# Kernel optimization log

Hardware: AMD Instinct MI355X
Metric: run time of the kernel (lower is better)

## Reference

```python
import jax, jax.numpy as jnp
import numpy as np

BETA = 0.95
THR = 1.0
SLOPE = 25.0


@jax.custom_vjp
def spike(x):
    # Heaviside spike with fast-sigmoid surrogate gradient (snntorch fast_sigmoid, slope=25)
    return (x > 0).astype(x.dtype)

def _spike_fwd(x):
    return spike(x), x

def _spike_bwd(x, g):
    sg = 1.0 / (SLOPE * jnp.abs(x) + 1.0) ** 2
    return (g * sg,)

spike.defvjp(_spike_fwd, _spike_bwd)


def setup_inputs() -> dict:
    key = jax.random.key(0)
    k_x, k_w1, k_b1, k_w2, k_b2 = jax.random.split(key, 5)
    T, B, D_IN, H, OUT = 30, 4096, 784, 128, 10
    x = jax.random.uniform(k_x, (T, B, D_IN), dtype=jnp.float32)
    # PyTorch nn.Linear default init: U(-1/sqrt(fan_in), 1/sqrt(fan_in))
    lim1 = 1.0 / np.sqrt(D_IN)
    lim2 = 1.0 / np.sqrt(H)
    W1 = jax.random.uniform(k_w1, (H, D_IN), jnp.float32, -lim1, lim1)
    b1 = jax.random.uniform(k_b1, (H,), jnp.float32, -lim1, lim1)
    W2 = jax.random.uniform(k_w2, (OUT, H), jnp.float32, -lim2, lim2)
    b2 = jax.random.uniform(k_b2, (OUT,), jnp.float32, -lim2, lim2)
    return {"x": x, "W1": W1, "b1": b1, "W2": W2, "b2": b2}


def reference(x, W1, b1, W2, b2):
    T, B, _ = x.shape
    H, OUT = W1.shape[0], W2.shape[0]

    def step(carry, xt):
        mem1, mem2 = carry
        # layer 1: linear + leaky integrate-and-fire (reset by subtraction)
        cur1 = xt @ W1.T + b1  # [B, H]
        reset1 = jax.lax.stop_gradient((mem1 - THR > 0).astype(xt.dtype))
        mem1 = BETA * mem1 + cur1 - reset1 * THR
        spk1 = spike(mem1 - THR)
        # layer 2
        cur2 = spk1 @ W2.T + b2  # [B, OUT]
        reset2 = jax.lax.stop_gradient((mem2 - THR > 0).astype(xt.dtype))
        mem2 = BETA * mem2 + cur2 - reset2 * THR
        spk2 = spike(mem2 - THR)
        return (mem1, mem2), (spk2, mem2)

    init = (jnp.zeros((B, H), x.dtype), jnp.zeros((B, OUT), x.dtype))
    _, (spk2_rec, mem2_rec) = jax.lax.scan(step, init, x)
    return spk2_rec, mem2_rec  # each [T, B, OUT]
```

## Files before the change

### kernel.cpp

```cpp
#include <hip/hip_runtime.h>
#include <stdint.h>

#define THR  1.0f
#define BETA 0.95f
#define SX   4096.0f
#define SW   512.0f
#define SINV (1.0f / (4096.0f * 512.0f))
#define W1N  (128 * 784)

typedef __attribute__((ext_vector_type(8)))  _Float16 f16x8;
typedef __attribute__((ext_vector_type(16))) float    f32x16;
typedef __attribute__((ext_vector_type(4)))  float    fvec4;

__device__ __forceinline__ void gll16(const float* g, float* l){
  __builtin_amdgcn_global_load_lds((const __attribute__((address_space(1))) void*)g,
                                   (__attribute__((address_space(3))) void*)l, 16, 0, 0);
}

__global__ void split_w1(const float* __restrict__ W1, _Float16* __restrict__ wB){
  int i = blockIdx.x * 256 + threadIdx.x;
  if (i < W1N) {
    int h = i / 784, k = i % 784;
    float v = W1[i] * SW;
    _Float16 hi = (_Float16)v;
    _Float16 lo = (_Float16)(v - (float)hi);
    int ks = k >> 4, kg = (k >> 3) & 1, j = k & 7, nf = h >> 5, r = h & 31;
    int base = ((ks * 4 + nf) * 2) * 512 + (kg * 32 + r) * 8 + j;
    wB[base]       = hi;
    wB[base + 512] = lo;
  }
}

__launch_bounds__(256, 2)
__global__ void gemm1(const float* __restrict__ x,
                      const float* __restrict__ wBf,
                      const float* __restrict__ b1,
                      float* __restrict__ cur1,
                      long row0){
  __shared__ float lds[20480];
  const int lane = threadIdx.x & 63;
  const int w    = threadIdx.x >> 6;
  const long blk_row0 = row0 + (long)blockIdx.x * 128;
  const int r  = lane & 31;
  const int kg = lane >> 5;

  const float* xA  = x + (blk_row0 + w * 32 + r) * 784 + kg * 8;
  const float* wBs = wBf + w * 512 + lane * 4;

  #define STAGE(bb, s) {                                                     \
    gll16(xA  + (s) * 16,         &lds[(bb) * 4096 + (w * 2 + 0) * 256]);    \
    gll16(xA  + (s) * 16 + 4,     &lds[(bb) * 4096 + (w * 2 + 1) * 256]);    \
    gll16(wBs + (s) * 2048,       &lds[(bb) * 4096 + 2048 + (w * 2 + 0) * 256]); \
    gll16(wBs + (s) * 2048 + 256, &lds[(bb) * 4096 + 2048 + (w * 2 + 1) * 256]); }

  #define CPH(bb) {                                                          \
    f16x8 b[8];                                                              \
    _Pragma("unroll") for (int f = 0; f < 8; ++f)                            \
      b[f] = *(const f16x8*)&lds[(bb) * 4096 + 2048 + f * 256 + lane * 4];   \
    fvec4 a0 = *(const fvec4*)&lds[(bb) * 4096 + (w * 2 + 0) * 256 + lane * 4]; \
    fvec4 a1 = *(const fvec4*)&lds[(bb) * 4096 + (w * 2 + 1) * 256 + lane * 4]; \
    f16x8 ah, al;                                                            \
    _Pragma("unroll") for (int j = 0; j < 8; ++j) {                          \
      float v = ((j < 4) ? a0[j] : a1[j - 4]) * SX;                          \
      _Float16 hh = (_Float16)v;                                             \
      ah[j] = hh; al[j] = (_Float16)(v - (float)hh);                         \
    }                                                                        \
    _Pragma("unroll") for (int nf = 0; nf < 4; ++nf) {                       \
      acc[nf] = __builtin_amdgcn_mfma_f32_32x32x16_f16(ah, b[nf * 2],     acc[nf], 0, 0, 0); \
      acc[nf] = __builtin_amdgcn_mfma_f32_32x32x16_f16(ah, b[nf * 2 + 1], acc[nf], 0, 0, 0); \
      acc[nf] = __builtin_amdgcn_mfma_f32_32x32x16_f16(al, b[nf * 2],     acc[nf], 0, 0, 0); \
    } }

  #define VMB(vm) {                                                          \
    asm volatile("s_waitcnt vmcnt(" #vm ")" ::: "memory");                   \
    __builtin_amdgcn_s_barrier();                                            \
    asm volatile("" ::: "memory");                                           \
    __builtin_amdgcn_sched_barrier(0); }

  f32x16 acc[4] = {};

  STAGE(0, 0); STAGE(1, 1); STAGE(2, 2);

  for (int g = 0; g < 9; ++g) {
    const int s5 = 5 * g;
    STAGE(3, s5 + 3); VMB(12); CPH(0);
    STAGE(4, s5 + 4); VMB(12); CPH(1);
    STAGE(0, s5 + 5); VMB(12); CPH(2);
    STAGE(1, s5 + 6); VMB(12); CPH(3);
    STAGE(2, s5 + 7); VMB(12); CPH(4);
  }
  STAGE(3, 48); VMB(12); CPH(0);
  VMB(8);  CPH(1);
  VMB(4);  CPH(2);
  VMB(0);  CPH(3);

  float b1v[4];
  #pragma unroll
  for (int nf = 0; nf < 4; ++nf) b1v[nf] = b1[nf * 32 + r];
  long m0 = (long)blockIdx.x * 128 + w * 32;
  #pragma unroll
  for (int nf = 0; nf < 4; ++nf)
    #pragma unroll
    for (int reg = 0; reg < 16; ++reg) {
      int rr = (reg & 3) + 8 * (reg >> 2) + 4 * kg;
      cur1[(m0 + rr) * 128 + nf * 32 + r] = acc[nf][reg] * SINV + b1v[nf];
    }
  #undef STAGE
  #undef CPH
  #undef VMB
}

__launch_bounds__(256)
__global__ void lif(const float* __restrict__ cur1,
                    const float* __restrict__ W2,
                    const float* __restrict__ b2,
                    float* __restrict__ out,
                    float* __restrict__ state1,
                    float* __restrict__ state2,
                    int t0, int tn){
  const int lane = threadIdx.x & 63;
  const int b = blockIdx.x * 4 + (threadIdx.x >> 6);
  const int o = lane & 15;
  const int c = lane >> 4;

  float wv[32];
  #pragma unroll
  for (int j = 0; j < 32; ++j) wv[j] = 0.f;
  if (o < 10) {
    #pragma unroll
    for (int j = 0; j < 32; ++j) wv[j] = W2[o * 128 + c * 32 + j];
  }
  float b2v = (lane < 10) ? b2[lane] : 0.f;

  float mem1a, mem1b, mem2;
  if (t0 == 0) { mem1a = 0.f; mem1b = 0.f; mem2 = 0.f; }
  else {
    mem1a = state1[b * 128 + lane];
    mem1b = state1[b * 128 + 64 + lane];
    mem2  = (lane < 10) ? state2[b * 10 + lane] : 0.f;
  }

  for (int t = t0; t < tn; ++t) {
    long base = ((long)(t - t0) * 4096 + b) * 128;
    float c1a = cur1[base + lane];
    float c1b = cur1[base + 64 + lane];
    float r1a = (mem1a > THR) ? THR : 0.f;
    float r1b = (mem1b > THR) ? THR : 0.f;
    mem1a = BETA * mem1a + c1a - r1a;
    mem1b = BETA * mem1b + c1b - r1b;

    uint64_t mA = __ballot(mem1a > THR);
    uint64_t mB = __ballot(mem1b > THR);
    uint64_t m64 = (c & 2) ? mB : mA;
    uint32_t bits = (uint32_t)(m64 >> ((c & 1) << 5));

    float s = 0.f;
    #pragma unroll
    for (int j = 0; j < 32; ++j)
      s = fmaf((float)((bits >> j) & 1u), wv[j], s);
    s += __shfl_xor(s, 16);
    s += __shfl_xor(s, 32);

    if (lane < 10) {
      float cur2 = s + b2v;
      float r2 = (mem2 > THR) ? THR : 0.f;
      mem2 = BETA * mem2 + cur2 - r2;
      float s2 = (mem2 > THR) ? 1.f : 0.f;
      long ob = (long)t * 40960 + (long)b * 10 + lane;
      out[ob] = s2;
      out[1228800 + ob] = mem2;
    }
  }

  if (tn < 30) {
    state1[b * 128 + lane] = mem1a;
    state1[b * 128 + 64 + lane] = mem1b;
    if (lane < 10) state2[b * 10 + lane] = mem2;
  }
}

extern "C" void kernel_launch(void* const* d_in, const int* in_sizes, int n_in,
                              void* d_out, int out_size, void* d_ws, size_t ws_size,
                              hipStream_t stream) {
  const float* x  = (const float*)d_in[0];
  const float* W1 = (const float*)d_in[1];
  const float* b1 = (const float*)d_in[2];
  const float* W2 = (const float*)d_in[3];
  const float* b2 = (const float*)d_in[4];
  float* out = (float*)d_out;

  const int T = 30, B = 4096;

  char* ws = (char*)d_ws;
  _Float16* wB = (_Float16*)ws;
  size_t off = (size_t)49 * 8 * 512 * sizeof(_Float16);
  off = (off + 255) & ~(size_t)255;
  float* state1 = (float*)(ws + off); off += (size_t)B * 128 * 4;
  float* state2 = (float*)(ws + off); off += (size_t)B * 10 * 4;
  off = (off + 255) & ~(size_t)255;
  float* cur1 = (float*)(ws + off);

  size_t per_t = (size_t)B * 128 * 4;
  size_t avail = (ws_size > off) ? (ws_size - off) : 0;
  int CH = (int)(avail / per_t);
  if (CH > T) CH = T;
  if (CH < 1) CH = 1;

  split_w1<<<(W1N + 255) / 256, 256, 0, stream>>>(W1, wB);

  for (int t0 = 0; t0 < T; t0 += CH) {
    int tn = (t0 + CH < T) ? (t0 + CH) : T;
    int mrows = (tn - t0) * B;
    gemm1<<<mrows / 128, 256, 0, stream>>>(x, (const float*)wB, b1, cur1, (long)t0 * B);
    lif<<<B / 4, 256, 0, stream>>>(cur1, W2, b2, out, state1, state2, t0, tn);
  }
}
```

Before: 171.1 us.

## Load W1 fragments directly to registers and drop block barriers in gemm1

The B operand (pre-split fp16 W1) is now loaded straight from global memory into double-buffered registers rather than staged through LDS. Each wave streams its own x tile into a private 4-slot LDS ring, so the per-step s_barrier across the block is gone and only vmcnt waits remain. This is meant to cut LDS traffic and barrier stalls, shrink shared memory, and possibly raise occupancy. In exchange every wave re-reads the same W1 fragments from global/L2 and holds more VGPRs, and the pipeline is shallower.

```diff
diff --git a/kernel.cpp b/kernel.cpp
--- a/kernel.cpp
+++ b/kernel.cpp
@@ -33,32 +33,34 @@
 
 __launch_bounds__(256, 2)
 __global__ void gemm1(const float* __restrict__ x,
-                      const float* __restrict__ wBf,
+                      const _Float16* __restrict__ wB,
                       const float* __restrict__ b1,
                       float* __restrict__ cur1,
                       long row0){
-  __shared__ float lds[20480];
+  __shared__ float lds[8192];
   const int lane = threadIdx.x & 63;
   const int w    = threadIdx.x >> 6;
   const long blk_row0 = row0 + (long)blockIdx.x * 128;
   const int r  = lane & 31;
   const int kg = lane >> 5;
 
-  const float* xA  = x + (blk_row0 + w * 32 + r) * 784 + kg * 8;
-  const float* wBs = wBf + w * 512 + lane * 4;
-
-  #define STAGE(bb, s) {                                                     \
-    gll16(xA  + (s) * 16,         &lds[(bb) * 4096 + (w * 2 + 0) * 256]);    \
-    gll16(xA  + (s) * 16 + 4,     &lds[(bb) * 4096 + (w * 2 + 1) * 256]);    \
-    gll16(wBs + (s) * 2048,       &lds[(bb) * 4096 + 2048 + (w * 2 + 0) * 256]); \
-    gll16(wBs + (s) * 2048 + 256, &lds[(bb) * 4096 + 2048 + (w * 2 + 1) * 256]); }
-
-  #define CPH(bb) {                                                          \
-    f16x8 b[8];                                                              \
-    _Pragma("unroll") for (int f = 0; f < 8; ++f)                            \
-      b[f] = *(const f16x8*)&lds[(bb) * 4096 + 2048 + f * 256 + lane * 4];   \
-    fvec4 a0 = *(const fvec4*)&lds[(bb) * 4096 + (w * 2 + 0) * 256 + lane * 4]; \
-    fvec4 a1 = *(const fvec4*)&lds[(bb) * 4096 + (w * 2 + 1) * 256 + lane * 4]; \
+  const float* xA = x + (blk_row0 + w * 32 + r) * 784 + kg * 8;
+  const f16x8* wv = (const f16x8*)wB + lane;
+  float* myl = &lds[w * 2048];
+
+  #define AST(bb, s) {                                                       \
+    gll16(xA + (s) * 16,     myl + (bb) * 512);                              \
+    gll16(xA + (s) * 16 + 4, myl + (bb) * 512 + 256); }
+
+  #define LDB(dst, s) { _Pragma("unroll") for (int f = 0; f < 8; ++f)        \
+      dst[f] = wv[((s) * 8 + f) * 64]; }
+
+  #define VMW(n) { asm volatile("s_waitcnt vmcnt(" #n ")" ::: "memory");     \
+                   __builtin_amdgcn_sched_barrier(0); }
+
+  #define CPH(bb, breg) {                                                    \
+    fvec4 a0 = *(const fvec4*)(myl + (bb) * 512 + lane * 4);                 \
+    fvec4 a1 = *(const fvec4*)(myl + (bb) * 512 + 256 + lane * 4);           \
     f16x8 ah, al;                                                            \
     _Pragma("unroll") for (int j = 0; j < 8; ++j) {                          \
       float v = ((j < 4) ? a0[j] : a1[j - 4]) * SX;                          \
@@ -66,33 +68,31 @@
       ah[j] = hh; al[j] = (_Float16)(v - (float)hh);                         \
     }                                                                        \
     _Pragma("unroll") for (int nf = 0; nf < 4; ++nf) {                       \
-      acc[nf] = __builtin_amdgcn_mfma_f32_32x32x16_f16(ah, b[nf * 2],     acc[nf], 0, 0, 0); \
-      acc[nf] = __builtin_amdgcn_mfma_f32_32x32x16_f16(ah, b[nf * 2 + 1], acc[nf], 0, 0, 0); \
-      acc[nf] = __builtin_amdgcn_mfma_f32_32x32x16_f16(al, b[nf * 2],     acc[nf], 0, 0, 0); \
+      acc[nf] = __builtin_amdgcn_mfma_f32_32x32x16_f16(ah, breg[nf * 2],     acc[nf], 0, 0, 0); \
+      acc[nf] = __builtin_amdgcn_mfma_f32_32x32x16_f16(ah, breg[nf * 2 + 1], acc[nf], 0, 0, 0); \
+      acc[nf] = __builtin_amdgcn_mfma_f32_32x32x16_f16(al, breg[nf * 2],     acc[nf], 0, 0, 0); \
     } }
 
-  #define VMB(vm) {                                                          \
-    asm volatile("s_waitcnt vmcnt(" #vm ")" ::: "memory");                   \
-    __builtin_amdgcn_s_barrier();                                            \
-    asm volatile("" ::: "memory");                                           \
-    __builtin_amdgcn_sched_barrier(0); }
+  #define STEP(s, bc, bn) {                                                  \
+    AST((s + 3) & 3, (s) + 3);                                               \
+    LDB(bn, (s) + 1);                                                        \
+    VMW(14);                                                                 \
+    CPH((s) & 3, bc); }
 
   f32x16 acc[4] = {};
-
-  STAGE(0, 0); STAGE(1, 1); STAGE(2, 2);
-
-  for (int g = 0; g < 9; ++g) {
-    const int s5 = 5 * g;
-    STAGE(3, s5 + 3); VMB(12); CPH(0);
-    STAGE(4, s5 + 4); VMB(12); CPH(1);
-    STAGE(0, s5 + 5); VMB(12); CPH(2);
-    STAGE(1, s5 + 6); VMB(12); CPH(3);
-    STAGE(2, s5 + 7); VMB(12); CPH(4);
-  }
-  STAGE(3, 48); VMB(12); CPH(0);
-  VMB(8);  CPH(1);
-  VMB(4);  CPH(2);
-  VMB(0);  CPH(3);
+  f16x8 bA[8], bB[8];
+
+  AST(0, 0); AST(1, 1); AST(2, 2);
+  LDB(bA, 0);
+
+  for (int s2 = 0; s2 < 23; ++s2) {
+    const int s = 2 * s2;
+    STEP(s,     bA, bB);
+    STEP(s + 1, bB, bA);
+  }
+  LDB(bB, 47); VMW(12); CPH(2, bA);
+  LDB(bA, 48); VMW(10); CPH(3, bB);
+  VMW(0); CPH(0, bA);
 
   float b1v[4];
   #pragma unroll
@@ -105,9 +105,11 @@
       int rr = (reg & 3) + 8 * (reg >> 2) + 4 * kg;
       cur1[(m0 + rr) * 128 + nf * 32 + r] = acc[nf][reg] * SINV + b1v[nf];
     }
-  #undef STAGE
+  #undef AST
+  #undef LDB
+  #undef VMW
   #undef CPH
-  #undef VMB
+  #undef STEP
 }
 
 __launch_bounds__(256)
@@ -211,7 +213,7 @@
   for (int t0 = 0; t0 < T; t0 += CH) {
     int tn = (t0 + CH < T) ? (t0 + CH) : T;
     int mrows = (tn - t0) * B;
-    gemm1<<<mrows / 128, 256, 0, stream>>>(x, (const float*)wB, b1, cur1, (long)t0 * B);
+    gemm1<<<mrows / 128, 256, 0, stream>>>(x, wB, b1, cur1, (long)t0 * B);
     lif<<<B / 4, 256, 0, stream>>>(cur1, W2, b2, out, state1, state2, t0, tn);
   }
 }
```

After: 216.6 us. 1.27x slower.

## Restructure GEMM1 pipeline to 32-wide K stages with split A/B buffering

Applied to the files above, without the earlier changes.

The GEMM1 main loop now stages 32 K-elements per stage instead of 16. It uses three A buffers and two B buffers in separate LDS regions, and the W1 tile is loaded cooperatively across waves. Each compute phase issues two K-steps, which halves the number of barrier/wait points per K. An lgkmcnt fence protects buffer reuse. The goal is less synchronisation overhead and better MFMA density, at the cost of fewer stages in flight and a more complex tail handling the odd final K-slice.

```diff
diff --git a/kernel.cpp b/kernel.cpp
--- a/kernel.cpp
+++ b/kernel.cpp
@@ -44,21 +44,30 @@
   const int r  = lane & 31;
   const int kg = lane >> 5;
 
-  const float* xA  = x + (blk_row0 + w * 32 + r) * 784 + kg * 8;
-  const float* wBs = wBf + w * 512 + lane * 4;
-
-  #define STAGE(bb, s) {                                                     \
-    gll16(xA  + (s) * 16,         &lds[(bb) * 4096 + (w * 2 + 0) * 256]);    \
-    gll16(xA  + (s) * 16 + 4,     &lds[(bb) * 4096 + (w * 2 + 1) * 256]);    \
-    gll16(wBs + (s) * 2048,       &lds[(bb) * 4096 + 2048 + (w * 2 + 0) * 256]); \
-    gll16(wBs + (s) * 2048 + 256, &lds[(bb) * 4096 + 2048 + (w * 2 + 1) * 256]); }
-
-  #define CPH(bb) {                                                          \
+  const float* xA = x + (blk_row0 + w * 32 + r) * 784 + kg * 8;
+
+  #define STAGE_A(aa, s) { _Pragma("unroll") for (int ksl = 0; ksl < 2; ++ksl) { \
+      gll16(xA + (s) * 32 + ksl * 16,     &lds[(aa) * 4096 + w * 1024 + ksl * 512]); \
+      gll16(xA + (s) * 32 + ksl * 16 + 4, &lds[(aa) * 4096 + w * 1024 + ksl * 512 + 256]); } }
+  #define STAGE_AT(aa) {                                                     \
+      gll16(xA + 768,     &lds[(aa) * 4096 + w * 1024]);                     \
+      gll16(xA + 768 + 4, &lds[(aa) * 4096 + w * 1024 + 256]); }
+
+  #define STAGE_B(bb, s) { _Pragma("unroll") for (int i = 0; i < 4; ++i) {   \
+      int j = w * 4 + i;                                                     \
+      gll16(wBf + (s) * 4096 + j * 256 + lane * 4,                           \
+            &lds[12288 + (bb) * 4096 + j * 256]); } }
+  #define STAGE_BT(bb) { _Pragma("unroll") for (int i = 0; i < 2; ++i) {     \
+      int j = w * 2 + i;                                                     \
+      gll16(wBf + 24 * 4096 + j * 256 + lane * 4,                            \
+            &lds[12288 + (bb) * 4096 + j * 256]); } }
+
+  #define KSTEP(aa, bb, ksl) {                                               \
     f16x8 b[8];                                                              \
     _Pragma("unroll") for (int f = 0; f < 8; ++f)                            \
-      b[f] = *(const f16x8*)&lds[(bb) * 4096 + 2048 + f * 256 + lane * 4];   \
-    fvec4 a0 = *(const fvec4*)&lds[(bb) * 4096 + (w * 2 + 0) * 256 + lane * 4]; \
-    fvec4 a1 = *(const fvec4*)&lds[(bb) * 4096 + (w * 2 + 1) * 256 + lane * 4]; \
+      b[f] = *(const f16x8*)&lds[12288 + (bb) * 4096 + ((ksl) * 8 + f) * 256 + lane * 4]; \
+    fvec4 a0 = *(const fvec4*)&lds[(aa) * 4096 + w * 1024 + (ksl) * 512 + lane * 4]; \
+    fvec4 a1 = *(const fvec4*)&lds[(aa) * 4096 + w * 1024 + (ksl) * 512 + 256 + lane * 4]; \
     f16x8 ah, al;                                                            \
     _Pragma("unroll") for (int j = 0; j < 8; ++j) {                          \
       float v = ((j < 4) ? a0[j] : a1[j - 4]) * SX;                          \
@@ -71,6 +80,12 @@
       acc[nf] = __builtin_amdgcn_mfma_f32_32x32x16_f16(al, b[nf * 2],     acc[nf], 0, 0, 0); \
     } }
 
+  #define CPH(aa, bb)  { KSTEP(aa, bb, 0); KSTEP(aa, bb, 1); }
+
+  #define FENCE_A() { __builtin_amdgcn_sched_barrier(0);                     \
+    asm volatile("s_waitcnt lgkmcnt(0)" ::: "memory");                       \
+    __builtin_amdgcn_s_barrier();                                            \
+    asm volatile("" ::: "memory"); }
   #define VMB(vm) {                                                          \
     asm volatile("s_waitcnt vmcnt(" #vm ")" ::: "memory");                   \
     __builtin_amdgcn_s_barrier();                                            \
@@ -79,20 +94,25 @@
 
   f32x16 acc[4] = {};
 
-  STAGE(0, 0); STAGE(1, 1); STAGE(2, 2);
-
-  for (int g = 0; g < 9; ++g) {
-    const int s5 = 5 * g;
-    STAGE(3, s5 + 3); VMB(12); CPH(0);
-    STAGE(4, s5 + 4); VMB(12); CPH(1);
-    STAGE(0, s5 + 5); VMB(12); CPH(2);
-    STAGE(1, s5 + 6); VMB(12); CPH(3);
-    STAGE(2, s5 + 7); VMB(12); CPH(4);
-  }
-  STAGE(3, 48); VMB(12); CPH(0);
-  VMB(8);  CPH(1);
-  VMB(4);  CPH(2);
-  VMB(0);  CPH(3);
+  STAGE_A(0, 0); STAGE_B(0, 0); STAGE_A(1, 1);
+
+  FENCE_A(); STAGE_B(1, 1); STAGE_A(2, 2); VMB(12); CPH(0, 0);
+
+  for (int g = 0; g < 3; ++g) {
+    const int s = 6 * g + 1;
+    FENCE_A(); STAGE_B(0, s + 1); STAGE_A(0, s + 2); VMB(12); CPH(1, 1);
+    FENCE_A(); STAGE_B(1, s + 2); STAGE_A(1, s + 3); VMB(12); CPH(2, 0);
+    FENCE_A(); STAGE_B(0, s + 3); STAGE_A(2, s + 4); VMB(12); CPH(0, 1);
+    FENCE_A(); STAGE_B(1, s + 4); STAGE_A(0, s + 5); VMB(12); CPH(1, 0);
+    FENCE_A(); STAGE_B(0, s + 5); STAGE_A(1, s + 6); VMB(12); CPH(2, 1);
+    FENCE_A(); STAGE_B(1, s + 6); STAGE_A(2, s + 7); VMB(12); CPH(0, 0);
+  }
+  FENCE_A(); STAGE_B(0, 20); STAGE_A(0, 21); VMB(12); CPH(1, 1);
+  FENCE_A(); STAGE_B(1, 21); STAGE_A(1, 22); VMB(12); CPH(2, 0);
+  FENCE_A(); STAGE_B(0, 22); STAGE_A(2, 23); VMB(12); CPH(0, 1);
+  FENCE_A(); STAGE_B(1, 23); STAGE_AT(0);    VMB(10); CPH(1, 0);
+  FENCE_A(); STAGE_BT(0);                    VMB(4);  CPH(2, 1);
+  FENCE_A();                                 VMB(0);  KSTEP(0, 0, 0);
 
   float b1v[4];
   #pragma unroll
@@ -105,8 +125,13 @@
       int rr = (reg & 3) + 8 * (reg >> 2) + 4 * kg;
       cur1[(m0 + rr) * 128 + nf * 32 + r] = acc[nf][reg] * SINV + b1v[nf];
     }
-  #undef STAGE
+  #undef STAGE_A
+  #undef STAGE_AT
+  #undef STAGE_B
+  #undef STAGE_BT
+  #undef KSTEP
   #undef CPH
+  #undef FENCE_A
   #undef VMB
 }
 
```

New measurement: 153.9 us. 10.0% less time.

## Restructure gemm1 pipeline to double-buffered 32-wide K stages with tail prefetch

Applied to the files above, without the earlier changes.

The GEMM1 main loop changes from a 5-deep ring of 16-wide K stages to 2 buffers, each holding 32 K values. The final 16-wide K slice is prefetched into its own LDS region at the start and processed after the loop. This halves the number of barrier and waitcnt points per K pass and issues more loads per stage. The cost is a shallower prefetch distance, which can leave memory latency exposed.

```diff
diff --git a/kernel.cpp b/kernel.cpp
--- a/kernel.cpp
+++ b/kernel.cpp
@@ -44,21 +44,25 @@
   const int r  = lane & 31;
   const int kg = lane >> 5;
 
-  const float* xA  = x + (blk_row0 + w * 32 + r) * 784 + kg * 8;
-  const float* wBs = wBf + w * 512 + lane * 4;
-
-  #define STAGE(bb, s) {                                                     \
-    gll16(xA  + (s) * 16,         &lds[(bb) * 4096 + (w * 2 + 0) * 256]);    \
-    gll16(xA  + (s) * 16 + 4,     &lds[(bb) * 4096 + (w * 2 + 1) * 256]);    \
-    gll16(wBs + (s) * 2048,       &lds[(bb) * 4096 + 2048 + (w * 2 + 0) * 256]); \
-    gll16(wBs + (s) * 2048 + 256, &lds[(bb) * 4096 + 2048 + (w * 2 + 1) * 256]); }
-
-  #define CPH(bb) {                                                          \
+  const float* xA = x + (blk_row0 + w * 32 + r) * 784 + kg * 8;
+
+  #define STAGE(p, s) {                                                      \
+    _Pragma("unroll") for (int ksl = 0; ksl < 2; ++ksl) {                    \
+      gll16(xA + (s) * 32 + ksl * 16,                                        \
+            &lds[(p) * 4096 + w * 1024 + ksl * 512]);                        \
+      gll16(xA + (s) * 32 + ksl * 16 + 4,                                    \
+            &lds[(p) * 4096 + w * 1024 + ksl * 512 + 256]); }                \
+    _Pragma("unroll") for (int i = 0; i < 4; ++i) {                          \
+      int j = w * 4 + i;                                                     \
+      gll16(wBf + (s) * 4096 + j * 256 + lane * 4,                           \
+            &lds[8192 + (p) * 4096 + j * 256]); } }
+
+  #define KSTEP(p, ksl) {                                                    \
     f16x8 b[8];                                                              \
     _Pragma("unroll") for (int f = 0; f < 8; ++f)                            \
-      b[f] = *(const f16x8*)&lds[(bb) * 4096 + 2048 + f * 256 + lane * 4];   \
-    fvec4 a0 = *(const fvec4*)&lds[(bb) * 4096 + (w * 2 + 0) * 256 + lane * 4]; \
-    fvec4 a1 = *(const fvec4*)&lds[(bb) * 4096 + (w * 2 + 1) * 256 + lane * 4]; \
+      b[f] = *(const f16x8*)&lds[8192 + (p) * 4096 + ((ksl) * 8 + f) * 256 + lane * 4]; \
+    fvec4 a0 = *(const fvec4*)&lds[(p) * 4096 + w * 1024 + (ksl) * 512 + lane * 4]; \
+    fvec4 a1 = *(const fvec4*)&lds[(p) * 4096 + w * 1024 + (ksl) * 512 + 256 + lane * 4]; \
     f16x8 ah, al;                                                            \
     _Pragma("unroll") for (int j = 0; j < 8; ++j) {                          \
       float v = ((j < 4) ? a0[j] : a1[j - 4]) * SX;                          \
@@ -71,6 +75,8 @@
       acc[nf] = __builtin_amdgcn_mfma_f32_32x32x16_f16(al, b[nf * 2],     acc[nf], 0, 0, 0); \
     } }
 
+  #define CPH(p) { KSTEP(p, 0); KSTEP(p, 1); }
+
   #define VMB(vm) {                                                          \
     asm volatile("s_waitcnt vmcnt(" #vm ")" ::: "memory");                   \
     __builtin_amdgcn_s_barrier();                                            \
@@ -79,20 +85,44 @@
 
   f32x16 acc[4] = {};
 
-  STAGE(0, 0); STAGE(1, 1); STAGE(2, 2);
-
-  for (int g = 0; g < 9; ++g) {
-    const int s5 = 5 * g;
-    STAGE(3, s5 + 3); VMB(12); CPH(0);
-    STAGE(4, s5 + 4); VMB(12); CPH(1);
-    STAGE(0, s5 + 5); VMB(12); CPH(2);
-    STAGE(1, s5 + 6); VMB(12); CPH(3);
-    STAGE(2, s5 + 7); VMB(12); CPH(4);
-  }
-  STAGE(3, 48); VMB(12); CPH(0);
-  VMB(8);  CPH(1);
-  VMB(4);  CPH(2);
-  VMB(0);  CPH(3);
+  gll16(xA + 768,     &lds[16384 + w * 512]);
+  gll16(xA + 768 + 4, &lds[16384 + w * 512 + 256]);
+  #pragma unroll
+  for (int i = 0; i < 2; ++i) {
+    int j = w * 2 + i;
+    gll16(wBf + 98304 + j * 256 + lane * 4, &lds[18432 + j * 256]);
+  }
+  STAGE(0, 0);
+
+  for (int q = 0; q < 11; ++q) {
+    const int s = 2 * q;
+    STAGE(1, s + 1); VMB(8); CPH(0);
+    STAGE(0, s + 2); VMB(8); CPH(1);
+  }
+  STAGE(1, 23); VMB(8); CPH(0);
+  VMB(0); CPH(1);
+
+  {
+    f16x8 b[8];
+    #pragma unroll
+    for (int f = 0; f < 8; ++f)
+      b[f] = *(const f16x8*)&lds[18432 + f * 256 + lane * 4];
+    fvec4 a0 = *(const fvec4*)&lds[16384 + w * 512 + lane * 4];
+    fvec4 a1 = *(const fvec4*)&lds[16384 + w * 512 + 256 + lane * 4];
+    f16x8 ah, al;
+    #pragma unroll
+    for (int j = 0; j < 8; ++j) {
+      float v = ((j < 4) ? a0[j] : a1[j - 4]) * SX;
+      _Float16 hh = (_Float16)v;
+      ah[j] = hh; al[j] = (_Float16)(v - (float)hh);
+    }
+    #pragma unroll
+    for (int nf = 0; nf < 4; ++nf) {
+      acc[nf] = __builtin_amdgcn_mfma_f32_32x32x16_f16(ah, b[nf * 2],     acc[nf], 0, 0, 0);
+      acc[nf] = __builtin_amdgcn_mfma_f32_32x32x16_f16(ah, b[nf * 2 + 1], acc[nf], 0, 0, 0);
+      acc[nf] = __builtin_amdgcn_mfma_f32_32x32x16_f16(al, b[nf * 2],     acc[nf], 0, 0, 0);
+    }
+  }
 
   float b1v[4];
   #pragma unroll
@@ -106,6 +136,7 @@
       cur1[(m0 + rr) * 128 + nf * 32 + r] = acc[nf][reg] * SINV + b1v[nf];
     }
   #undef STAGE
+  #undef KSTEP
   #undef CPH
   #undef VMB
 }
```

After: 155.8 us. 1.1x faster.
